# Optimization experiments

Hardware: AMD Instinct MI355X
Metric: run time of the kernel (lower is better)

Reference implementation:

```python
import jax, jax.numpy as jnp
import numpy as np

N_MENTIONS = 4096
N_PAIRS = 32768
N_SEGMENTS = 1024  # number of spans (ragged softmax groups)
G_DIM = 3 * 768    # span representation dim (3*embed_dim)
D_IN = 3 * G_DIM + 20
HIDDEN = 150


def setup_inputs() -> dict:
    key = jax.random.key(0)
    ks = jax.random.split(key, 11)
    inp = {
        "g_i": jax.random.normal(ks[0], (N_MENTIONS, G_DIM), jnp.float32),
        "mention_scores": jax.random.normal(ks[1], (N_MENTIONS, 1), jnp.float32),
        "speaker_embed": jax.random.normal(ks[2], (3, 20), jnp.float32) * 0.02,
        "W1": jax.random.normal(ks[3], (D_IN, HIDDEN), jnp.float32) * (1.0 / np.sqrt(D_IN)),
        "b1": jnp.zeros((HIDDEN,), jnp.float32),
        "W2": jax.random.normal(ks[4], (HIDDEN, 1), jnp.float32) * (1.0 / np.sqrt(HIDDEN)),
        "b2": jnp.zeros((1,), jnp.float32),
        "mention_ids": jax.random.randint(ks[5], (N_PAIRS,), 0, N_MENTIONS),
        "antecedent_ids": jax.random.randint(ks[6], (N_PAIRS,), 0, N_MENTIONS),
        "speaker_labels": jax.random.randint(ks[7], (N_PAIRS,), 0, 3),
        "segment_ids": jnp.sort(jax.random.randint(ks[8], (N_PAIRS,), 0, N_SEGMENTS)),
    }
    return inp


def reference(g_i, mention_scores, speaker_embed, W1, b1, W2, b2,
              mention_ids, antecedent_ids, speaker_labels, segment_ids):
    # Gather mention / antecedent span representations. [P, G]
    i_g = g_i[mention_ids]
    j_g = g_i[antecedent_ids]
    phi = speaker_embed[speaker_labels]  # [P, speaker_dim]

    # Pair features: cat(i_g, j_g, i_g*j_g, phi). [P, D_IN]
    pairs = jnp.concatenate([i_g, j_g, i_g * j_g, phi], axis=1)

    # Score MLP: Linear -> ReLU -> Linear(->1). (dropout off in eval)
    h = jax.nn.relu(pairs @ W1 + b1)          # [P, HIDDEN]
    s_ij = (h @ W2 + b2)[:, 0]                # [P]

    # coref score = s_i + s_j + s_ij
    s_i = mention_scores[mention_ids, 0]
    s_j = mention_scores[antecedent_ids, 0]
    scores = s_i + s_j + s_ij                 # [P]

    # Ragged per-span softmax with an appended epsilon logit of 0.0.
    seg_max = jax.ops.segment_max(scores, segment_ids, num_segments=N_SEGMENTS)
    m = jnp.maximum(seg_max, 0.0)             # include epsilon=0 in the max
    e = jnp.exp(scores - m[segment_ids])      # [P]
    eps_e = jnp.exp(-m)                       # [S] exp(0 - m)
    denom = jax.ops.segment_sum(e, segment_ids, num_segments=N_SEGMENTS) + eps_e
    pair_probs = e / denom[segment_ids]       # [P]
    eps_probs = eps_e / denom                 # [S]

    # Flattened: all pair probs followed by the per-span epsilon probs.
    return jnp.concatenate([pair_probs, eps_probs])
```

## Files before the change

### kernel.cpp

```cpp
#include <hip/hip_runtime.h>
#include <cstdint>

#define NM   4096
#define NP   32768
#define NSEG 1024
#define GD   2304
#define HID  150
#define NPAD 160
#define KG32 72
#define SEG_ELEMS (KG32 * 10 * 512)

typedef unsigned short u16;
typedef short s16x8 __attribute__((ext_vector_type(8)));
typedef float f32x4 __attribute__((ext_vector_type(4)));
typedef uint32_t u32x4 __attribute__((ext_vector_type(4)));

union Frag {
    uint32_t u[4];
    s16x8    v;
};

__device__ inline uint32_t cvtpk(float lo, float hi) {
    uint32_t r;
    asm("v_cvt_pk_bf16_f32 %0, %1, %2" : "=v"(r) : "v"(lo), "v"(hi));
    return r;
}

__device__ inline f32x4 mfma16(s16x8 a, s16x8 b, f32x4 c) {
    return __builtin_amdgcn_mfma_f32_16x16x32_bf16(a, b, c, 0, 0, 0);
}

__device__ inline s16x8 prodpack(u32x4 iu, u32x4 ju) {
    Frag f;
#pragma unroll
    for (int m = 0; m < 4; ++m) {
        uint32_t x = iu[m], y = ju[m];
        float lo = __builtin_bit_cast(float, x << 16) *
                   __builtin_bit_cast(float, y << 16);
        float hi = __builtin_bit_cast(float, x & 0xffff0000u) *
                   __builtin_bit_cast(float, y & 0xffff0000u);
        f.u[m] = cvtpk(lo, hi);
    }
    return f.v;
}

__launch_bounds__(256)
__global__ void prep_kernel(const float* __restrict__ W1,
                            const float* __restrict__ spk,
                            const float* __restrict__ b1,
                            const float* __restrict__ W2,
                            const int* __restrict__ mids,
                            u16* __restrict__ wpack,
                            float* __restrict__ phib,
                            float* __restrict__ w2pad,
                            int* __restrict__ cnt) {
    const int b = blockIdx.x;
    if (b < 540) {
        int idx = b * 256 + threadIdx.x;
        int lane = idx & 63;
        int t    = idx >> 6;
        int nf   = t % 10;
        int sk   = t / 10;
        int seg  = sk / KG32, kg = sk % KG32;
        int kbase = (seg == 0) ? 2 * GD : ((seg == 1) ? 0 : GD);
        int n    = nf * 16 + (lane & 15);
        int krow = kbase + kg * 32 + ((lane >> 4) << 3);
        u32x4 d = (u32x4){0u, 0u, 0u, 0u};
        if (n < HID) {
#pragma unroll
            for (int jj = 0; jj < 4; ++jj) {
                float v0 = W1[(size_t)(krow + 2 * jj) * HID + n];
                float v1 = W1[(size_t)(krow + 2 * jj + 1) * HID + n];
                d[jj] = cvtpk(v0, v1);
            }
        }
        *(u32x4*)(wpack + (size_t)idx * 8) = d;
    } else if (b < 543) {
        int t = (b - 540) * 256 + threadIdx.x;
        if (t < 3 * NPAD) {
            int s = t / NPAD, n = t - s * NPAD;
            float a = 0.f;
            if (n < HID) {
                for (int d = 0; d < 20; ++d)
                    a = fmaf(spk[s * 20 + d], W1[(size_t)(3 * GD + d) * HID + n], a);
                a += b1[n];
            }
            phib[t] = a;
        } else if (t < 4 * NPAD) {
            int n = t - 3 * NPAD;
            w2pad[n] = (n < HID) ? W2[n] : 0.f;
        }
    } else {
        int p = (b - 543) * 256 + threadIdx.x;
        if (p < NP) atomicAdd(&cnt[mids[p]], 1);
    }
}

__global__ __launch_bounds__(1024)
void sort_scan_kernel(int* __restrict__ cnt, int* __restrict__ bas) {
    __shared__ int lsum[1024];
    const int t = threadIdx.x;
    int v[4];
    int s = 0;
#pragma unroll
    for (int j = 0; j < 4; ++j) { v[j] = cnt[4 * t + j]; s += v[j]; }
    int val = s;
    lsum[t] = val;
    __syncthreads();
    for (int off = 1; off < 1024; off <<= 1) {
        int x = (t >= off) ? lsum[t - off] : 0;
        __syncthreads();
        val += x;
        lsum[t] = val;
        __syncthreads();
    }
    int run = val - s;
#pragma unroll
    for (int j = 0; j < 4; ++j) {
        bas[4 * t + j] = run;
        run += v[j];
        cnt[4 * t + j] = 0;
    }
}

struct A2 { f32x4 x0, x1; };

__launch_bounds__(256)
__global__ void gemm_pre_kernel(const float* __restrict__ gi,
                                const u16* __restrict__ wpackIJ,
                                u16* __restrict__ gbf,
                                float* __restrict__ APre,
                                const int* __restrict__ mids,
                                const int* __restrict__ bas,
                                int* __restrict__ cnt,
                                int* __restrict__ perm) {
    const int blk = blockIdx.x;
    __shared__ float xch[3][64][44];

    if (blk >= 512) {
        int p = (blk - 512) * 256 + threadIdx.x;
        if (p < NP) {
            int m = mids[p];
            int pos = bas[m] + atomicAdd(&cnt[m], 1);
            perm[pos] = p;
        }
        return;
    }

    const int tid = threadIdx.x;
    const int kh = tid >> 6, lane = tid & 63;
    const int quad = lane >> 4, l15 = lane & 15;
    const int mt = blk & 255, ng = blk >> 8;
    const u16* wp = wpackIJ + (size_t)ng * SEG_ELEMS + lane * 8;
    const int row = mt * 16 + l15;

    f32x4 acc[10];
#pragma unroll
    for (int b = 0; b < 10; ++b) acc[b] = (f32x4){0.f, 0.f, 0.f, 0.f};

    const float* ap = gi + (size_t)row * GD + quad * 8;
    u16* gb = gbf + (size_t)row * GD + quad * 8;
    const bool emit = (ng == 0);
    const int u0 = kh * 18;

    A2 a0, a1, a2;
    Frag b0[10], b1[10];

#define LDA(ax, k) { ax.x0 = *(const f32x4*)(ap + (u0 + (k)) * 32); \
                     ax.x1 = *(const f32x4*)(ap + (u0 + (k)) * 32 + 4); }
#define LDBP(bb, k) { const u16* wn = wp + (size_t)(u0 + (k)) * 5120; \
        _Pragma("unroll") for (int nf = 0; nf < 10; ++nf) \
            bb[nf].v = *(const s16x8*)(const void*)(wn + nf * 512); }
#define PHP(k, ax, bb) { \
        Frag a; \
        a.u[0] = cvtpk(ax.x0[0], ax.x0[1]); a.u[1] = cvtpk(ax.x0[2], ax.x0[3]); \
        a.u[2] = cvtpk(ax.x1[0], ax.x1[1]); a.u[3] = cvtpk(ax.x1[2], ax.x1[3]); \
        if (emit) *(u32x4*)(gb + (u0 + (k)) * 32) = *(const u32x4*)a.u; \
        _Pragma("unroll") for (int nf = 0; nf < 10; ++nf) \
            acc[nf] = mfma16(a.v, bb[nf].v, acc[nf]); }

    LDBP(b0, 0); LDBP(b1, 1);
    LDA(a0, 0); LDA(a1, 1); LDA(a2, 2);

#pragma unroll 1
    for (int t = 0; t < 2; ++t) {
        const int kb = t * 6;
        PHP(kb + 0, a0, b0); LDBP(b0, kb + 2); LDA(a0, kb + 3);
        PHP(kb + 1, a1, b1); LDBP(b1, kb + 3); LDA(a1, kb + 4);
        PHP(kb + 2, a2, b0); LDBP(b0, kb + 4); LDA(a2, kb + 5);
        PHP(kb + 3, a0, b1); LDBP(b1, kb + 5); LDA(a0, kb + 6);
        PHP(kb + 4, a1, b0); LDBP(b0, kb + 6); LDA(a1, kb + 7);
        PHP(kb + 5, a2, b1); LDBP(b1, kb + 7); LDA(a2, kb + 8);
    }
    PHP(12, a0, b0); LDBP(b0, 14); LDA(a0, 15);
    PHP(13, a1, b1); LDBP(b1, 15); LDA(a1, 16);
    PHP(14, a2, b0); LDBP(b0, 16); LDA(a2, 17);
    PHP(15, a0, b1); LDBP(b1, 17);
    PHP(16, a1, b0);
    PHP(17, a2, b1);

#undef LDA
#undef LDBP
#undef PHP

    if (kh != 0) {
        float* dst = &xch[kh - 1][lane][0];
#pragma unroll
        for (int nf = 0; nf < 10; ++nf)
            *(f32x4*)(dst + nf * 4) = acc[nf];
    }
    __syncthreads();
    if (kh == 0) {
#pragma unroll
        for (int k = 0; k < 3; ++k) {
            const float* src = &xch[k][lane][0];
#pragma unroll
            for (int nf = 0; nf < 10; ++nf)
                acc[nf] += *(const f32x4*)(src + nf * 4);
        }
        const int colbase = ng * NPAD + l15;
        float* Ap = APre + (size_t)(mt * 16 + quad * 4) * 320 + colbase;
#pragma unroll
        for (int nf = 0; nf < 10; ++nf)
#pragma unroll
            for (int r = 0; r < 4; ++r)
                Ap[(size_t)r * 320 + nf * 16] = acc[nf][r];
    }
}

struct G4 { u32x4 i0, j0, i1, j1; };

__launch_bounds__(128)
__global__ void gemm_pairs_kernel(const u16* __restrict__ gbf,
                                  const u16* __restrict__ wpackP,
                                  const float* __restrict__ APre,
                                  const float* __restrict__ phib,
                                  const float* __restrict__ w2pad,
                                  const float* __restrict__ mscore,
                                  const float* __restrict__ b2,
                                  const int* __restrict__ mids,
                                  const int* __restrict__ aids,
                                  const int* __restrict__ slab,
                                  const int* __restrict__ perm,
                                  float* __restrict__ scores) {
    const int tid = threadIdx.x;
    const int wave = tid >> 6, lane = tid & 63;
    const int quad = lane >> 4, l15 = lane & 15;
    const int base = blockIdx.x * 64 + wave * 32;

    f32x4 acc[2][10];
#pragma unroll
    for (int a = 0; a < 2; ++a)
#pragma unroll
        for (int b = 0; b < 10; ++b) acc[a][b] = (f32x4){0.f, 0.f, 0.f, 0.f};

    const int p0 = perm[base + l15], p1 = perm[base + 16 + l15];
    const u16* ip0 = gbf + (size_t)mids[p0] * GD + quad * 8;
    const u16* jp0 = gbf + (size_t)aids[p0] * GD + quad * 8;
    const u16* ip1 = gbf + (size_t)mids[p1] * GD + quad * 8;
    const u16* jp1 = gbf + (size_t)aids[p1] * GD + quad * 8;
    const u16* wl = wpackP + lane * 8;

    G4 g0, g1, g2;
    Frag b0[10], b1[10];

#define LDG(g, k) { const int off = (k) * 32; \
        g.i0 = *(const u32x4*)(ip0 + off); g.j0 = *(const u32x4*)(jp0 + off); \
        g.i1 = *(const u32x4*)(ip1 + off); g.j1 = *(const u32x4*)(jp1 + off); }
#define LDB(bb, k) { const u16* wn = wl + (size_t)(k) * 5120; \
        _Pragma("unroll") for (int nf = 0; nf < 10; ++nf) \
            bb[nf].v = *(const s16x8*)(const void*)(wn + nf * 512); }
#define PH(g, bb) { \
        s16x8 a0 = prodpack(g.i0, g.j0); \
        s16x8 a1 = prodpack(g.i1, g.j1); \
        _Pragma("unroll") for (int nf = 0; nf < 10; ++nf) { \
            acc[0][nf] = mfma16(a0, bb[nf].v, acc[0][nf]); \
            acc[1][nf] = mfma16(a1, bb[nf].v, acc[1][nf]); } }

    LDG(g0, 0); LDG(g1, 1); LDG(g2, 2);
    LDB(b0, 0); LDB(b1, 1);

#pragma unroll 1
    for (int t = 0; t < 11; ++t) {
        const int kb = t * 6;
        PH(g0, b0); LDG(g0, kb + 3); LDB(b0, kb + 2);
        PH(g1, b1); LDG(g1, kb + 4); LDB(b1, kb + 3);
        PH(g2, b0); LDG(g2, kb + 5); LDB(b0, kb + 4);
        PH(g0, b1); LDG(g0, kb + 6); LDB(b1, kb + 5);
        PH(g1, b0); LDG(g1, kb + 7); LDB(b0, kb + 6);
        PH(g2, b1); LDG(g2, kb + 8); LDB(b1, kb + 7);
    }
    PH(g0, b0); LDG(g0, 69); LDB(b0, 68);
    PH(g1, b1); LDG(g1, 70); LDB(b1, 69);
    PH(g2, b0); LDG(g2, 71); LDB(b0, 70);
    PH(g0, b1); LDB(b1, 71);
    PH(g1, b0);
    PH(g2, b1);

#undef LDG
#undef LDB
#undef PH

    float w2v[10];
#pragma unroll
    for (int nf = 0; nf < 10; ++nf) w2v[nf] = w2pad[nf * 16 + l15];
    const float b2v = b2[0];

#pragma unroll
    for (int mf = 0; mf < 2; ++mf)
#pragma unroll
        for (int r = 0; r < 4; ++r) {
            const int p  = perm[base + mf * 16 + quad * 4 + r];
            const int mi = mids[p], ai = aids[p], sp = slab[p];
            const float* Ai = APre + (size_t)mi * 320;
            const float* Bj = APre + (size_t)ai * 320 + NPAD;
            const float* Ph = phib + sp * NPAD;
            float partial = 0.f;
#pragma unroll
            for (int nf = 0; nf < 10; ++nf) {
                const int c = nf * 16 + l15;
                float h = acc[mf][nf][r] + Ai[c] + Bj[c] + Ph[c];
                h = fmaxf(h, 0.f);
                partial = fmaf(h, w2v[nf], partial);
            }
            partial += __shfl_xor(partial, 1);
            partial += __shfl_xor(partial, 2);
            partial += __shfl_xor(partial, 4);
            partial += __shfl_xor(partial, 8);
            if (l15 == 0)
                scores[p] = partial + b2v + mscore[mi] + mscore[ai];
        }
}

__global__ void seg_softmax_kernel(const float* __restrict__ scores,
                                   const int* __restrict__ seg,
                                   float* __restrict__ out) {
    const int s = blockIdx.x;
    const int lane = threadIdx.x;
    int lo = 0, hi = NP;
    while (lo < hi) { int mid = (lo + hi) >> 1; if (seg[mid] < s) lo = mid + 1; else hi = mid; }
    const int start = lo;
    int lo2 = start, hi2 = NP;
    while (lo2 < hi2) { int mid = (lo2 + hi2) >> 1; if (seg[mid] <= s) lo2 = mid + 1; else hi2 = mid; }
    const int end = lo2;

    float m = 0.f;
    for (int i = start + lane; i < end; i += 64) m = fmaxf(m, scores[i]);
#pragma unroll
    for (int msk = 1; msk < 64; msk <<= 1) m = fmaxf(m, __shfl_xor(m, msk));

    float sum = 0.f;
    for (int i = start + lane; i < end; i += 64) sum += __expf(scores[i] - m);
#pragma unroll
    for (int msk = 1; msk < 64; msk <<= 1) sum += __shfl_xor(sum, msk);

    const float epse = __expf(-m);
    const float inv  = 1.f / (sum + epse);
    for (int i = start + lane; i < end; i += 64) out[i] = __expf(scores[i] - m) * inv;
    if (lane == 0) out[NP + s] = epse * inv;
}

extern "C" void kernel_launch(void* const* d_in, const int* in_sizes, int n_in,
                              void* d_out, int out_size, void* d_ws, size_t ws_size,
                              hipStream_t stream) {
    const float* gi     = (const float*)d_in[0];
    const float* mscore = (const float*)d_in[1];
    const float* spk    = (const float*)d_in[2];
    const float* W1     = (const float*)d_in[3];
    const float* b1     = (const float*)d_in[4];
    const float* W2     = (const float*)d_in[5];
    const float* b2     = (const float*)d_in[6];
    const int*   mids   = (const int*)d_in[7];
    const int*   aids   = (const int*)d_in[8];
    const int*   slab   = (const int*)d_in[9];
    const int*   segs   = (const int*)d_in[10];
    float* out = (float*)d_out;

    char* w = (char*)d_ws;
    u16*   gbf    = (u16*)w;
    u16*   wpack  = (u16*)(w + 18874368);
    float* APre   = (float*)(w + 21086208);
    float* scores = (float*)(w + 26329088);
    float* phib   = (float*)(w + 26460160);
    float* w2pad  = (float*)(w + 26462080);
    int*   cnt    = (int*)(w + 26462720);
    int*   bas    = (int*)(w + 26479104);
    int*   perm   = (int*)(w + 26495488);

    hipMemsetAsync(cnt, 0, NM * sizeof(int), stream);
    prep_kernel<<<dim3(671), dim3(256), 0, stream>>>(W1, spk, b1, W2, mids,
                                                     wpack, phib, w2pad, cnt);
    sort_scan_kernel<<<dim3(1), dim3(1024), 0, stream>>>(cnt, bas);
    gemm_pre_kernel<<<dim3(640), dim3(256), 0, stream>>>(gi, wpack + SEG_ELEMS, gbf, APre,
                                                         mids, bas, cnt, perm);
    gemm_pairs_kernel<<<dim3(512), dim3(128), 0, stream>>>(gbf, wpack, APre, phib, w2pad,
                                                           mscore, b2, mids, aids, slab,
                                                           perm, scores);
    seg_softmax_kernel<<<dim3(NSEG), dim3(64), 0, stream>>>(scores, segs, out);
}
```

Baseline: 198.6 us.

## Split gemm_pre K across 8 waves with half-width B prefetch; merge softmax bound searches

gemm_pre_kernel now uses 512 threads, so eight waves each handle 9 K-steps instead of four waves doing 18. The partial sums are reduced through a larger shared buffer. Each step loads B in two 5-fragment halves interleaved with the MFMAs, which cuts register pressure so more waves can be resident and hide latency, at the cost of a heavier shared-memory reduction. The softmax kernel finds the segment start and end with one binary search per lane (even lanes search s, odd lanes s+1) and broadcasts the results, instead of running two searches in sequence.

Result: slower. 218.3 us (+9.9%).

```diff
diff --git a/kernel.cpp b/kernel.cpp
--- a/kernel.cpp
+++ b/kernel.cpp
@@ -125,7 +125,7 @@
 
 struct A2 { f32x4 x0, x1; };
 
-__launch_bounds__(256)
+__launch_bounds__(512, 4)
 __global__ void gemm_pre_kernel(const float* __restrict__ gi,
                                 const u16* __restrict__ wpackIJ,
                                 u16* __restrict__ gbf,
@@ -135,10 +135,8 @@
                                 int* __restrict__ cnt,
                                 int* __restrict__ perm) {
     const int blk = blockIdx.x;
-    __shared__ float xch[3][64][44];
-
     if (blk >= 512) {
-        int p = (blk - 512) * 256 + threadIdx.x;
+        int p = (blk - 512) * 512 + threadIdx.x;
         if (p < NP) {
             int m = mids[p];
             int pos = bas[m] + atomicAdd(&cnt[m], 1);
@@ -146,6 +144,8 @@
         }
         return;
     }
+
+    __shared__ float xch[7][64][44];
 
     const int tid = threadIdx.x;
     const int kh = tid >> 6, lane = tid & 63;
@@ -161,47 +161,40 @@
     const float* ap = gi + (size_t)row * GD + quad * 8;
     u16* gb = gbf + (size_t)row * GD + quad * 8;
     const bool emit = (ng == 0);
-    const int u0 = kh * 18;
-
-    A2 a0, a1, a2;
-    Frag b0[10], b1[10];
+    const int u0 = kh * 9;
+
+    A2 a0, a1;
+    Frag bE[5], bO[5], apk;
 
 #define LDA(ax, k) { ax.x0 = *(const f32x4*)(ap + (u0 + (k)) * 32); \
                      ax.x1 = *(const f32x4*)(ap + (u0 + (k)) * 32 + 4); }
-#define LDBP(bb, k) { const u16* wn = wp + (size_t)(u0 + (k)) * 5120; \
-        _Pragma("unroll") for (int nf = 0; nf < 10; ++nf) \
+#define LDB5(bb, k, hf) { const u16* wn = wp + (size_t)(u0 + (k)) * 5120 + (hf) * 2560; \
+        _Pragma("unroll") for (int nf = 0; nf < 5; ++nf) \
             bb[nf].v = *(const s16x8*)(const void*)(wn + nf * 512); }
-#define PHP(k, ax, bb) { \
-        Frag a; \
-        a.u[0] = cvtpk(ax.x0[0], ax.x0[1]); a.u[1] = cvtpk(ax.x0[2], ax.x0[3]); \
-        a.u[2] = cvtpk(ax.x1[0], ax.x1[1]); a.u[3] = cvtpk(ax.x1[2], ax.x1[3]); \
-        if (emit) *(u32x4*)(gb + (u0 + (k)) * 32) = *(const u32x4*)a.u; \
-        _Pragma("unroll") for (int nf = 0; nf < 10; ++nf) \
-            acc[nf] = mfma16(a.v, bb[nf].v, acc[nf]); }
-
-    LDBP(b0, 0); LDBP(b1, 1);
-    LDA(a0, 0); LDA(a1, 1); LDA(a2, 2);
-
-#pragma unroll 1
-    for (int t = 0; t < 2; ++t) {
-        const int kb = t * 6;
-        PHP(kb + 0, a0, b0); LDBP(b0, kb + 2); LDA(a0, kb + 3);
-        PHP(kb + 1, a1, b1); LDBP(b1, kb + 3); LDA(a1, kb + 4);
-        PHP(kb + 2, a2, b0); LDBP(b0, kb + 4); LDA(a2, kb + 5);
-        PHP(kb + 3, a0, b1); LDBP(b1, kb + 5); LDA(a0, kb + 6);
-        PHP(kb + 4, a1, b0); LDBP(b0, kb + 6); LDA(a1, kb + 7);
-        PHP(kb + 5, a2, b1); LDBP(b1, kb + 7); LDA(a2, kb + 8);
-    }
-    PHP(12, a0, b0); LDBP(b0, 14); LDA(a0, 15);
-    PHP(13, a1, b1); LDBP(b1, 15); LDA(a1, 16);
-    PHP(14, a2, b0); LDBP(b0, 16); LDA(a2, 17);
-    PHP(15, a0, b1); LDBP(b1, 17);
-    PHP(16, a1, b0);
-    PHP(17, a2, b1);
+#define PACKA(ax) { \
+        apk.u[0] = cvtpk(ax.x0[0], ax.x0[1]); apk.u[1] = cvtpk(ax.x0[2], ax.x0[3]); \
+        apk.u[2] = cvtpk(ax.x1[0], ax.x1[1]); apk.u[3] = cvtpk(ax.x1[2], ax.x1[3]); }
+#define STEP(s, ax) { \
+        PACKA(ax); \
+        if (emit) *(u32x4*)(gb + (u0 + (s)) * 32) = *(const u32x4*)apk.u; \
+        _Pragma("unroll") for (int nf = 0; nf < 5; ++nf) \
+            acc[nf] = mfma16(apk.v, bE[nf].v, acc[nf]); \
+        if ((s) < 8) LDB5(bE, (s) + 1, 0); \
+        if ((s) < 7) LDA(ax, (s) + 2); \
+        _Pragma("unroll") for (int nf = 0; nf < 5; ++nf) \
+            acc[5 + nf] = mfma16(apk.v, bO[nf].v, acc[5 + nf]); \
+        if ((s) < 8) LDB5(bO, (s) + 1, 1); }
+
+    LDB5(bE, 0, 0); LDB5(bO, 0, 1);
+    LDA(a0, 0); LDA(a1, 1);
+
+    STEP(0, a0); STEP(1, a1); STEP(2, a0); STEP(3, a1); STEP(4, a0);
+    STEP(5, a1); STEP(6, a0); STEP(7, a1); STEP(8, a0);
 
 #undef LDA
-#undef LDBP
-#undef PHP
+#undef LDB5
+#undef PACKA
+#undef STEP
 
     if (kh != 0) {
         float* dst = &xch[kh - 1][lane][0];
@@ -212,7 +205,7 @@
     __syncthreads();
     if (kh == 0) {
 #pragma unroll
-        for (int k = 0; k < 3; ++k) {
+        for (int k = 0; k < 7; ++k) {
             const float* src = &xch[k][lane][0];
 #pragma unroll
             for (int nf = 0; nf < 10; ++nf)
@@ -337,12 +330,12 @@
                                    float* __restrict__ out) {
     const int s = blockIdx.x;
     const int lane = threadIdx.x;
+
+    const int tgt = s + (lane & 1);
     int lo = 0, hi = NP;
-    while (lo < hi) { int mid = (lo + hi) >> 1; if (seg[mid] < s) lo = mid + 1; else hi = mid; }
-    const int start = lo;
-    int lo2 = start, hi2 = NP;
-    while (lo2 < hi2) { int mid = (lo2 + hi2) >> 1; if (seg[mid] <= s) lo2 = mid + 1; else hi2 = mid; }
-    const int end = lo2;
+    while (lo < hi) { int mid = (lo + hi) >> 1; if (seg[mid] < tgt) lo = mid + 1; else hi = mid; }
+    const int start = __shfl(lo, 0);
+    const int end   = __shfl(lo, 1);
 
     float m = 0.f;
     for (int i = start + lane; i < end; i += 64) m = fmaxf(m, scores[i]);
@@ -391,7 +384,7 @@
     prep_kernel<<<dim3(671), dim3(256), 0, stream>>>(W1, spk, b1, W2, mids,
                                                      wpack, phib, w2pad, cnt);
     sort_scan_kernel<<<dim3(1), dim3(1024), 0, stream>>>(cnt, bas);
-    gemm_pre_kernel<<<dim3(640), dim3(256), 0, stream>>>(gi, wpack + SEG_ELEMS, gbf, APre,
+    gemm_pre_kernel<<<dim3(576), dim3(512), 0, stream>>>(gi, wpack + SEG_ELEMS, gbf, APre,
                                                          mids, bas, cnt, perm);
     gemm_pairs_kernel<<<dim3(512), dim3(128), 0, stream>>>(gbf, wpack, APre, phib, w2pad,
                                                            mscore, b2, mids, aids, slab,
```
